# Performance work log

Measured on AMD Instinct MI355X. Metric: run time of the kernel, lower is better.

## Reference

```python
import jax, jax.numpy as jnp
import numpy as np

HEAD_DIM = 64
SCALE = HEAD_DIM ** -0.5
NEG_INF = jnp.finfo(jnp.float32).min


def setup_inputs() -> dict:
    key = jax.random.key(0)
    kq, kk, kv = jax.random.split(key, 3)
    shape = (4, 16, 2048, HEAD_DIM)  # [batch, heads, seq, head_dim]
    return {
        "q": jax.random.normal(kq, shape, dtype=jnp.float32),
        "k": jax.random.normal(kk, shape, dtype=jnp.float32),
        "v": jax.random.normal(kv, shape, dtype=jnp.float32),
    }


def reference(q, k, v):
    # similarity = QK^T * scale, shape [b, h, i, j]
    sim = jnp.einsum("bhid,bhjd->bhij", q, k) * SCALE
    seq_len = sim.shape[-1]
    # causal mask: disallow j > i
    causal = jnp.triu(jnp.ones((seq_len, seq_len), dtype=bool), k=1)
    sim = jnp.where(causal, NEG_INF, sim)
    attn = jax.nn.softmax(sim, axis=-1)
    out = jnp.einsum("bhij,bhjd->bhid", attn, v)
    return out
```

## Files before the change

### kernel.cpp

```cpp
#include <hip/hip_runtime.h>
#include <hip/hip_bf16.h>

#define SEQ 2048
#define HD 64
#define NQB (SEQ / 128)

typedef __bf16 bf16x8 __attribute__((ext_vector_type(8)));
typedef float f32x4 __attribute__((ext_vector_type(4)));
typedef float f32x16 __attribute__((ext_vector_type(16)));
typedef unsigned int u32x4 __attribute__((ext_vector_type(4)));

typedef const __attribute__((address_space(1))) void gvoid_t;
typedef __attribute__((address_space(3))) void svoid_t;

__device__ __forceinline__ void gload_lds16(const void* g, void* l) {
  __builtin_amdgcn_global_load_lds((gvoid_t*)g, (svoid_t*)l, 16, 0, 0);
}

__device__ __forceinline__ bf16x8 cvt8(const float* p) {
  float4 a = *(const float4*)p;
  float4 b = *(const float4*)(p + 4);
  bf16x8 w;
  w[0] = (__bf16)a.x; w[1] = (__bf16)a.y; w[2] = (__bf16)a.z; w[3] = (__bf16)a.w;
  w[4] = (__bf16)b.x; w[5] = (__bf16)b.y; w[6] = (__bf16)b.z; w[7] = (__bf16)b.w;
  return w;
}

__device__ __forceinline__ unsigned cvtpk_bf16(float lo, float hi) {
  unsigned r;
  asm("v_cvt_pk_bf16_f32 %0, %1, %2" : "=v"(r) : "v"(lo), "v"(hi));
  return r;
}

__device__ __forceinline__ float tmax16(const f32x16& v) {
  float a0 = fmaxf(v[0], v[1]), a1 = fmaxf(v[2], v[3]);
  float a2 = fmaxf(v[4], v[5]), a3 = fmaxf(v[6], v[7]);
  float a4 = fmaxf(v[8], v[9]), a5 = fmaxf(v[10], v[11]);
  float a6 = fmaxf(v[12], v[13]), a7 = fmaxf(v[14], v[15]);
  float b0 = fmaxf(a0, a1), b1 = fmaxf(a2, a3), b2 = fmaxf(a4, a5), b3 = fmaxf(a6, a7);
  return fmaxf(fmaxf(b0, b1), fmaxf(b2, b3));
}

__global__ void prep_kernel(const float* __restrict__ K,
                            const float* __restrict__ V,
                            unsigned short* __restrict__ Kswz,
                            unsigned short* __restrict__ Vt) {
  __shared__ __align__(16) unsigned short sT[64 * 72];
  const int t = threadIdx.x;
  const int kb = blockIdx.x;
  const int bh = blockIdx.y;
  const int j0 = kb * 64;
  const size_t ibase = (size_t)bh * SEQ * HD;

  {
    const int j = t >> 2;
    const int m = (t & 3) * 2;
    const float* src = K + ibase + (size_t)(j0 + j) * HD + m * 8;
    unsigned short* dst = Kswz + ibase + (size_t)(j0 + j) * HD;
#pragma unroll
    for (int h = 0; h < 2; ++h) {
      bf16x8 w = cvt8(src + 8 * h);
      const int c = (m + h) ^ (j & 7);
      *(bf16x8*)(dst + c * 8) = w;
    }
  }
  {
    const int jr = t >> 2;
    const int d0 = (t & 3) * 16;
    const float* vsrc = V + ibase + (size_t)(j0 + jr) * HD + d0;
#pragma unroll
    for (int h = 0; h < 4; ++h) {
      float4 a = *(const float4*)(vsrc + 4 * h);
      sT[(d0 + 4 * h + 0) * 72 + jr] = __builtin_bit_cast(unsigned short, (__bf16)a.x);
      sT[(d0 + 4 * h + 1) * 72 + jr] = __builtin_bit_cast(unsigned short, (__bf16)a.y);
      sT[(d0 + 4 * h + 2) * 72 + jr] = __builtin_bit_cast(unsigned short, (__bf16)a.z);
      sT[(d0 + 4 * h + 3) * 72 + jr] = __builtin_bit_cast(unsigned short, (__bf16)a.w);
    }
  }
  __syncthreads();
  {
#pragma unroll
    for (int p = 0; p < 2; ++p) {
      const int cid = t + 256 * p;
      const int d = cid >> 3;
      const int jj = cid & 7;
      bf16x8 w = *(const bf16x8*)(&sT[d * 72 + 8 * jj]);
      const int c = jj ^ (d & 7);
      *(bf16x8*)(Vt + (size_t)bh * HD * SEQ + (size_t)d * SEQ + j0 + c * 8) = w;
    }
  }
}

__global__ __launch_bounds__(256, 2) void fattn_kernel(
    const float* __restrict__ Q, const unsigned short* __restrict__ Kswz,
    const unsigned short* __restrict__ Vt, float* __restrict__ O) {
  __shared__ __align__(16) unsigned short sbuf[3][2 * 64 * 64];

  const int tid = threadIdx.x;
  const int wid = tid >> 6;
  const int lane = tid & 63;
  const int l31 = lane & 31;
  const int hi = lane >> 5;

  const int p = blockIdx.x;
  const int qbA = p;
  const int qbB = NQB - 1 - p;
  const int bh = blockIdx.y;

  const int i0A = qbA * 128 + wid * 32;
  const int i0B = qbB * 128 + wid * 32;
  const int igA = i0A + l31;
  const int igB = i0B + l31;

  const float* Qp = Q + (size_t)bh * SEQ * HD;
  const unsigned short* Kg = Kswz + (size_t)bh * SEQ * HD;
  const unsigned short* Vg = Vt + (size_t)bh * HD * SEQ;
  float* Op = O + (size_t)bh * SEQ * HD;

  const float qscale = 0.125f * 1.44269504088896340736f;
  bf16x8 qfA[4], qfB[4];
#pragma unroll
  for (int grp = 0; grp < 2; ++grp) {
    const float* qr = Qp + (size_t)(grp ? igB : igA) * HD + 8 * hi;
#pragma unroll
    for (int c = 0; c < 4; ++c) {
      float4 a = *(const float4*)(qr + 16 * c);
      float4 b = *(const float4*)(qr + 16 * c + 4);
      bf16x8 w;
      w[0] = (__bf16)(a.x * qscale); w[1] = (__bf16)(a.y * qscale);
      w[2] = (__bf16)(a.z * qscale); w[3] = (__bf16)(a.w * qscale);
      w[4] = (__bf16)(b.x * qscale); w[5] = (__bf16)(b.y * qscale);
      w[6] = (__bf16)(b.z * qscale); w[7] = (__bf16)(b.w * qscale);
      if (grp) qfB[c] = w; else qfA[c] = w;
    }
  }

  f32x16 z16;
#pragma unroll
  for (int r = 0; r < 16; ++r) z16[r] = 0.f;

  f32x16 oAl, oBl, oAh, oBh;
#pragma unroll
  for (int r = 0; r < 16; ++r) { oAl[r] = 0.f; oBl[r] = 0.f; oAh[r] = 0.f; oBh[r] = 0.f; }
  float mA = -1e30f, lA = 0.f, mB = -1e30f, lB = 0.f;

  const int nkb = 2 * qbB + 2;
  const int kbLowMax = 2 * qbA + 1;

  auto stage = [&](int buf, int j0s) {
    unsigned short* bK = &sbuf[buf][0];
    unsigned short* bV = &sbuf[buf][4096];
#pragma unroll
    for (int tt = 0; tt < 2; ++tt) {
      const int row = 16 * wid + 8 * tt;
      const unsigned short* gk =
          Kg + (size_t)(j0s + row + (lane >> 3)) * HD + (lane & 7) * 8;
      gload_lds16(gk, bK + row * HD);
      const unsigned short* gv =
          Vg + (size_t)(row + (lane >> 3)) * SEQ + j0s + (lane & 7) * 8;
      gload_lds16(gv, bV + row * HD);
    }
  };

  const int swz = (l31 & 7) << 4;

  stage(0, 0);
  stage(1, 64);

  for (int kb = 0; kb < nkb; ++kb) {
    const int j0 = kb * 64;
    if (kb + 1 < nkb) {
      asm volatile("s_waitcnt vmcnt(4)" ::: "memory");
    } else {
      asm volatile("s_waitcnt vmcnt(0)" ::: "memory");
    }
    __builtin_amdgcn_s_barrier();
    __builtin_amdgcn_sched_barrier(0);
    if (kb + 2 < nkb) stage((kb + 2) % 3, j0 + 128);

    const unsigned short* bK = &sbuf[kb % 3][0];
    const unsigned short* bV = &sbuf[kb % 3][4096];
    const bool lowAct = (kb <= kbLowMax);

    f32x16 sAl, sBl, sAh, sBh;

    __builtin_amdgcn_s_setprio(1);
    {
      const int boff = (16 * hi) ^ swz;
      bf16x8 kf0 = *(const bf16x8*)((const char*)bK + l31 * 128 + boff);
      bf16x8 kf1 = *(const bf16x8*)((const char*)bK + (32 + l31) * 128 + boff);
      sAh = __builtin_amdgcn_mfma_f32_32x32x16_bf16(kf0, qfB[0], z16, 0, 0, 0);
      sBh = __builtin_amdgcn_mfma_f32_32x32x16_bf16(kf1, qfB[0], z16, 0, 0, 0);
      if (lowAct) {
        sAl = __builtin_amdgcn_mfma_f32_32x32x16_bf16(kf0, qfA[0], z16, 0, 0, 0);
        sBl = __builtin_amdgcn_mfma_f32_32x32x16_bf16(kf1, qfA[0], z16, 0, 0, 0);
      } else {
        sAl = z16; sBl = z16;
      }
    }
#pragma unroll
    for (int c = 1; c < 4; ++c) {
      const int boff = (32 * c + 16 * hi) ^ swz;
      bf16x8 kf0 = *(const bf16x8*)((const char*)bK + l31 * 128 + boff);
      bf16x8 kf1 = *(const bf16x8*)((const char*)bK + (32 + l31) * 128 + boff);
      sAh = __builtin_amdgcn_mfma_f32_32x32x16_bf16(kf0, qfB[c], sAh, 0, 0, 0);
      sBh = __builtin_amdgcn_mfma_f32_32x32x16_bf16(kf1, qfB[c], sBh, 0, 0, 0);
      if (lowAct) {
        sAl = __builtin_amdgcn_mfma_f32_32x32x16_bf16(kf0, qfA[c], sAl, 0, 0, 0);
        sBl = __builtin_amdgcn_mfma_f32_32x32x16_bf16(kf1, qfA[c], sBl, 0, 0, 0);
      }
    }
    __builtin_amdgcn_s_setprio(0);

    if (j0 + 63 > i0B) {
#pragma unroll
      for (int r = 0; r < 16; ++r) {
        const int jl = j0 + (r & 3) + 8 * (r >> 2) + 4 * hi;
        sAh[r] = (jl <= igB) ? sAh[r] : -1e30f;
        sBh[r] = (jl + 32 <= igB) ? sBh[r] : -1e30f;
      }
    }
    if (lowAct && (j0 + 63 > i0A)) {
#pragma unroll
      for (int r = 0; r < 16; ++r) {
        const int jl = j0 + (r & 3) + 8 * (r >> 2) + 4 * hi;
        sAl[r] = (jl <= igA) ? sAl[r] : -1e30f;
        sBl[r] = (jl + 32 <= igA) ? sBl[r] : -1e30f;
      }
    }

    bf16x8 pfh[4], pfl[4];

#define MKFRAG(SV, BASE, DST)                                                \
    {                                                                        \
      unsigned a0 = cvtpk_bf16(SV[BASE + 0], SV[BASE + 1]);                  \
      unsigned b0 = cvtpk_bf16(SV[BASE + 4], SV[BASE + 5]);                  \
      asm("v_permlane32_swap_b32 %0, %1" : "+v"(a0), "+v"(b0));              \
      unsigned a1 = cvtpk_bf16(SV[BASE + 2], SV[BASE + 3]);                  \
      unsigned b1 = cvtpk_bf16(SV[BASE + 6], SV[BASE + 7]);                  \
      asm("v_permlane32_swap_b32 %0, %1" : "+v"(a1), "+v"(b1));              \
      u32x4 wv = {a0, a1, b0, b1};                                           \
      DST = __builtin_bit_cast(bf16x8, wv);                                  \
    }

#define SOFTMAX_FRAG(SA, SB, MRUN, LRUN, OA, OB, PFR)                        \
    {                                                                        \
      float pmax = fmaxf(tmax16(SA), tmax16(SB));                            \
      pmax = fmaxf(pmax, __shfl_xor(pmax, 32));                              \
      if (!__all(pmax - MRUN <= 10.0f)) {                                    \
        const float mn = fmaxf(MRUN, pmax);                                  \
        const float al = __builtin_amdgcn_exp2f(MRUN - mn);                  \
        MRUN = mn;                                                           \
        LRUN *= al;                                                          \
        _Pragma("unroll")                                                    \
        for (int r = 0; r < 16; ++r) { OA[r] *= al; OB[r] *= al; }           \
      }                                                                      \
      float rs0 = 0.f, rs1 = 0.f, rs2 = 0.f, rs3 = 0.f;                      \
      _Pragma("unroll")                                                      \
      for (int r = 0; r < 4; ++r) {                                          \
        SA[4 * r + 0] = __builtin_amdgcn_exp2f(SA[4 * r + 0] - MRUN);        \
        SA[4 * r + 1] = __builtin_amdgcn_exp2f(SA[4 * r + 1] - MRUN);        \
        SA[4 * r + 2] = __builtin_amdgcn_exp2f(SA[4 * r + 2] - MRUN);        \
        SA[4 * r + 3] = __builtin_amdgcn_exp2f(SA[4 * r + 3] - MRUN);        \
        rs0 += SA[4 * r + 0]; rs1 += SA[4 * r + 1];                          \
        rs2 += SA[4 * r + 2]; rs3 += SA[4 * r + 3];                          \
      }                                                                      \
      _Pragma("unroll")                                                      \
      for (int r = 0; r < 4; ++r) {                                          \
        SB[4 * r + 0] = __builtin_amdgcn_exp2f(SB[4 * r + 0] - MRUN);        \
        SB[4 * r + 1] = __builtin_amdgcn_exp2f(SB[4 * r + 1] - MRUN);        \
        SB[4 * r + 2] = __builtin_amdgcn_exp2f(SB[4 * r + 2] - MRUN);        \
        SB[4 * r + 3] = __builtin_amdgcn_exp2f(SB[4 * r + 3] - MRUN);        \
        rs0 += SB[4 * r + 0]; rs1 += SB[4 * r + 1];                          \
        rs2 += SB[4 * r + 2]; rs3 += SB[4 * r + 3];                          \
      }                                                                      \
      float rs = (rs0 + rs1) + (rs2 + rs3);                                  \
      rs += __shfl_xor(rs, 32);                                              \
      LRUN += rs;                                                            \
      MKFRAG(SA, 0, PFR[0]) MKFRAG(SA, 8, PFR[1])                            \
      MKFRAG(SB, 0, PFR[2]) MKFRAG(SB, 8, PFR[3])                            \
    }

    SOFTMAX_FRAG(sAh, sBh, mB, lB, oAh, oBh, pfh)
    if (lowAct) {
      SOFTMAX_FRAG(sAl, sBl, mA, lA, oAl, oBl, pfl)
    }
#undef SOFTMAX_FRAG
#undef MKFRAG

    __builtin_amdgcn_s_setprio(1);
    if (lowAct) {
#pragma unroll
      for (int ks = 0; ks < 4; ++ks) {
        const int vbo = (32 * ks + 16 * hi) ^ swz;
        bf16x8 vf0 = *(const bf16x8*)((const char*)bV + l31 * 128 + vbo);
        bf16x8 vf1 = *(const bf16x8*)((const char*)bV + (32 + l31) * 128 + vbo);
        oAh = __builtin_amdgcn_mfma_f32_32x32x16_bf16(vf0, pfh[ks], oAh, 0, 0, 0);
        oBh = __builtin_amdgcn_mfma_f32_32x32x16_bf16(vf1, pfh[ks], oBh, 0, 0, 0);
        oAl = __builtin_amdgcn_mfma_f32_32x32x16_bf16(vf0, pfl[ks], oAl, 0, 0, 0);
        oBl = __builtin_amdgcn_mfma_f32_32x32x16_bf16(vf1, pfl[ks], oBl, 0, 0, 0);
      }
    } else {
#pragma unroll
      for (int ks = 0; ks < 4; ++ks) {
        const int vbo = (32 * ks + 16 * hi) ^ swz;
        bf16x8 vf0 = *(const bf16x8*)((const char*)bV + l31 * 128 + vbo);
        bf16x8 vf1 = *(const bf16x8*)((const char*)bV + (32 + l31) * 128 + vbo);
        oAh = __builtin_amdgcn_mfma_f32_32x32x16_bf16(vf0, pfh[ks], oAh, 0, 0, 0);
        oBh = __builtin_amdgcn_mfma_f32_32x32x16_bf16(vf1, pfh[ks], oBh, 0, 0, 0);
      }
    }
    __builtin_amdgcn_s_setprio(0);
  }

#pragma unroll
  for (int grp = 0; grp < 2; ++grp) {
    const float inv = 1.f / (grp ? lB : lA);
    float* orow = Op + (size_t)(grp ? igB : igA) * HD;
    const f32x16& xA = grp ? oAh : oAl;
    const f32x16& xB = grp ? oBh : oBl;
#pragma unroll
    for (int q2 = 0; q2 < 4; ++q2) {
      float4 o;
      o.x = xA[4 * q2 + 0] * inv; o.y = xA[4 * q2 + 1] * inv;
      o.z = xA[4 * q2 + 2] * inv; o.w = xA[4 * q2 + 3] * inv;
      *(float4*)(orow + 8 * q2 + 4 * hi) = o;
      float4 pq;
      pq.x = xB[4 * q2 + 0] * inv; pq.y = xB[4 * q2 + 1] * inv;
      pq.z = xB[4 * q2 + 2] * inv; pq.w = xB[4 * q2 + 3] * inv;
      *(float4*)(orow + 32 + 8 * q2 + 4 * hi) = pq;
    }
  }
}

__global__ void fattn_fallback(const float* __restrict__ Q,
                               const float* __restrict__ K,
                               const float* __restrict__ V,
                               float* __restrict__ O) {
  __shared__ __align__(16) unsigned short sK[64 * 64];
  __shared__ __align__(16) unsigned short sVt[64 * 72];
  __shared__ __align__(16) unsigned short sP[4][16 * 72];

  const int tid = threadIdx.x;
  const int wid = tid >> 6;
  const int lane = tid & 63;
  const int g = lane >> 4;
  const int lx = lane & 15;

  const int qb = (int)gridDim.x - 1 - (int)blockIdx.x;
  const int bh = blockIdx.y;
  const int q0 = qb * 64;

  const size_t base = (size_t)bh * SEQ * HD;
  const float* Qp = Q + base;
  const float* Kp = K + base;
  const float* Vp = V + base;
  float* Op = O + base;

  bf16x8 qf[2];
  {
    const int row = q0 + wid * 16 + lx;
    const float* qr = Qp + (size_t)row * HD + 8 * g;
#pragma unroll
    for (int c = 0; c < 2; ++c) {
      float4 a = *(const float4*)(qr + 32 * c);
      float4 b = *(const float4*)(qr + 32 * c + 4);
      bf16x8 w;
      w[0] = (__bf16)(a.x * 0.125f); w[1] = (__bf16)(a.y * 0.125f);
      w[2] = (__bf16)(a.z * 0.125f); w[3] = (__bf16)(a.w * 0.125f);
      w[4] = (__bf16)(b.x * 0.125f); w[5] = (__bf16)(b.y * 0.125f);
      w[6] = (__bf16)(b.z * 0.125f); w[7] = (__bf16)(b.w * 0.125f);
      qf[c] = w;
    }
  }

  f32x4 acc[4];
#pragma unroll
  for (int dt = 0; dt < 4; ++dt) acc[dt] = (f32x4){0.f, 0.f, 0.f, 0.f};
  float m_run[4], l_run[4];
#pragma unroll
  for (int r = 0; r < 4; ++r) { m_run[r] = -1e30f; l_run[r] = 0.f; }

  const int iw0 = q0 + wid * 16;
  const int nkb = qb + 1;

  for (int kb = 0; kb < nkb; ++kb) {
    const int j0 = kb * 64;
    __syncthreads();
    {
      const int jr = tid >> 2;
      const int d0 = (tid & 3) * 16;
      const float* src = Kp + (size_t)(j0 + jr) * HD + d0;
#pragma unroll
      for (int h = 0; h < 2; ++h) {
        bf16x8 w = cvt8(src + 8 * h);
        const int byteoff = ((d0 + 8 * h) * 2) ^ ((jr & 7) << 4);
        *(bf16x8*)((char*)sK + jr * 128 + byteoff) = w;
      }
      const float* vsrc = Vp + (size_t)(j0 + jr) * HD + d0;
#pragma unroll
      for (int h = 0; h < 4; ++h) {
        float4 a = *(const float4*)(vsrc + 4 * h);
        sVt[(d0 + 4 * h + 0) * 72 + jr] = __builtin_bit_cast(unsigned short, (__bf16)a.x);
        sVt[(d0 + 4 * h + 1) * 72 + jr] = __builtin_bit_cast(unsigned short, (__bf16)a.y);
        sVt[(d0 + 4 * h + 2) * 72 + jr] = __builtin_bit_cast(unsigned short, (__bf16)a.z);
        sVt[(d0 + 4 * h + 3) * 72 + jr] = __builtin_bit_cast(unsigned short, (__bf16)a.w);
      }
    }
    __syncthreads();

    float s[4][4];
#pragma unroll
    for (int jt = 0; jt < 4; ++jt) {
      f32x4 c = (f32x4){0.f, 0.f, 0.f, 0.f};
#pragma unroll
      for (int cc = 0; cc < 2; ++cc) {
        const int row = jt * 16 + lx;
        const int byteoff = (16 * g + 64 * cc) ^ ((row & 7) << 4);
        bf16x8 kf = *(const bf16x8*)((const char*)sK + row * 128 + byteoff);
        c = __builtin_amdgcn_mfma_f32_16x16x32_bf16(qf[cc], kf, c, 0, 0, 0);
      }
      const int jg = j0 + jt * 16 + lx;
#pragma unroll
      for (int r = 0; r < 4; ++r) {
        const int igf = iw0 + 4 * g + r;
        s[jt][r] = (jg <= igf) ? c[r] : -1e30f;
      }
    }

#pragma unroll
    for (int r = 0; r < 4; ++r) {
      float mt = fmaxf(fmaxf(s[0][r], s[1][r]), fmaxf(s[2][r], s[3][r]));
#pragma unroll
      for (int msk = 1; msk <= 8; msk <<= 1) mt = fmaxf(mt, __shfl_xor(mt, msk));
      const float mn = fmaxf(m_run[r], mt);
      const float alpha = __expf(m_run[r] - mn);
      m_run[r] = mn;
      float rs = 0.f;
#pragma unroll
      for (int jt = 0; jt < 4; ++jt) {
        const float pv = __expf(s[jt][r] - mn);
        s[jt][r] = pv;
        rs += pv;
      }
#pragma unroll
      for (int msk = 1; msk <= 8; msk <<= 1) rs += __shfl_xor(rs, msk);
      l_run[r] = l_run[r] * alpha + rs;
#pragma unroll
      for (int dt = 0; dt < 4; ++dt) acc[dt][r] *= alpha;
    }

#pragma unroll
    for (int jt = 0; jt < 4; ++jt)
#pragma unroll
      for (int r = 0; r < 4; ++r)
        sP[wid][(4 * g + r) * 72 + jt * 16 + lx] =
            __builtin_bit_cast(unsigned short, (__bf16)s[jt][r]);
    asm volatile("s_waitcnt lgkmcnt(0)" ::: "memory");

#pragma unroll
    for (int cc = 0; cc < 2; ++cc) {
      bf16x8 pf = *(const bf16x8*)(&sP[wid][lx * 72 + 8 * g + 32 * cc]);
#pragma unroll
      for (int dt = 0; dt < 4; ++dt) {
        bf16x8 vf = *(const bf16x8*)(&sVt[(lx + 16 * dt) * 72 + 8 * g + 32 * cc]);
        acc[dt] = __builtin_amdgcn_mfma_f32_16x16x32_bf16(pf, vf, acc[dt], 0, 0, 0);
      }
    }
  }

#pragma unroll
  for (int r = 0; r < 4; ++r) {
    const float inv = 1.f / l_run[r];
    const int igf = q0 + wid * 16 + 4 * g + r;
    float* orow = Op + (size_t)igf * HD + lx;
#pragma unroll
    for (int dt = 0; dt < 4; ++dt) orow[16 * dt] = acc[dt][r] * inv;
  }
}

extern "C" void kernel_launch(void* const* d_in, const int* in_sizes, int n_in,
                              void* d_out, int out_size, void* d_ws, size_t ws_size,
                              hipStream_t stream) {
  const float* q = (const float*)d_in[0];
  const float* k = (const float*)d_in[1];
  const float* v = (const float*)d_in[2];
  float* o = (float*)d_out;

  const size_t kv_elems = (size_t)64 * SEQ * HD;
  const size_t need = 2 * kv_elems * sizeof(unsigned short);

  if (ws_size >= need) {
    unsigned short* kswz = (unsigned short*)d_ws;
    unsigned short* vt = kswz + kv_elems;
    dim3 pgrid(SEQ / 64, 64);
    prep_kernel<<<pgrid, 256, 0, stream>>>(k, v, kswz, vt);
    dim3 grid(NQB / 2, 64);
    fattn_kernel<<<grid, 256, 0, stream>>>(q, kswz, vt, o);
  } else {
    dim3 grid(SEQ / 64, 64);
    fattn_fallback<<<grid, 256, 0, stream>>>(q, k, v, o);
  }
}
```

Measured before the change: 88.88 us.

## Process two KV tiles per barrier with a four-slot LDS ring

The KV loop changes from one 64-key tile per iteration with a 3-buffer ring to two tiles per iteration with a 4-buffer ring. Each iteration waits for all outstanding loads, issues loads for the next two tiles, then processes two tiles. This halves the number of barriers and waitcnt points, at the cost of more LDS (64KB per block) and a full vmcnt(0) wait each iteration, which may lower occupancy and reduce how well loads overlap with compute.

```diff
diff --git a/kernel.cpp b/kernel.cpp
--- a/kernel.cpp
+++ b/kernel.cpp
@@ -94,7 +94,7 @@
 __global__ __launch_bounds__(256, 2) void fattn_kernel(
     const float* __restrict__ Q, const unsigned short* __restrict__ Kswz,
     const unsigned short* __restrict__ Vt, float* __restrict__ O) {
-  __shared__ __align__(16) unsigned short sbuf[3][2 * 64 * 64];
+  __shared__ __align__(16) unsigned short sbuf[4][2 * 64 * 64];
 
   const int tid = threadIdx.x;
   const int wid = tid >> 6;
@@ -144,43 +144,31 @@
   for (int r = 0; r < 16; ++r) { oAl[r] = 0.f; oBl[r] = 0.f; oAh[r] = 0.f; oBh[r] = 0.f; }
   float mA = -1e30f, lA = 0.f, mB = -1e30f, lB = 0.f;
 
-  const int nkb = 2 * qbB + 2;
-  const int kbLowMax = 2 * qbA + 1;
-
-  auto stage = [&](int buf, int j0s) {
-    unsigned short* bK = &sbuf[buf][0];
-    unsigned short* bV = &sbuf[buf][4096];
+  const int totTiles = 2 * qbB + 2;
+  const int nIter = qbB + 1;
+
+  auto stage = [&](int tile) {
+    unsigned short* base = &sbuf[0][0] + (size_t)(tile & 3) * 8192;
+    const int j0s = tile * 64;
 #pragma unroll
     for (int tt = 0; tt < 2; ++tt) {
       const int row = 16 * wid + 8 * tt;
       const unsigned short* gk =
           Kg + (size_t)(j0s + row + (lane >> 3)) * HD + (lane & 7) * 8;
-      gload_lds16(gk, bK + row * HD);
+      gload_lds16(gk, base + row * HD);
       const unsigned short* gv =
           Vg + (size_t)(row + (lane >> 3)) * SEQ + j0s + (lane & 7) * 8;
-      gload_lds16(gv, bV + row * HD);
+      gload_lds16(gv, base + 4096 + row * HD);
     }
   };
 
   const int swz = (l31 & 7) << 4;
 
-  stage(0, 0);
-  stage(1, 64);
-
-  for (int kb = 0; kb < nkb; ++kb) {
-    const int j0 = kb * 64;
-    if (kb + 1 < nkb) {
-      asm volatile("s_waitcnt vmcnt(4)" ::: "memory");
-    } else {
-      asm volatile("s_waitcnt vmcnt(0)" ::: "memory");
-    }
-    __builtin_amdgcn_s_barrier();
-    __builtin_amdgcn_sched_barrier(0);
-    if (kb + 2 < nkb) stage((kb + 2) % 3, j0 + 128);
-
-    const unsigned short* bK = &sbuf[kb % 3][0];
-    const unsigned short* bV = &sbuf[kb % 3][4096];
-    const bool lowAct = (kb <= kbLowMax);
+  auto processTile = [&](int tile, bool dual) {
+    const int j0 = tile * 64;
+    const unsigned short* base = &sbuf[0][0] + (size_t)(tile & 3) * 8192;
+    const unsigned short* bK = base;
+    const unsigned short* bV = base + 4096;
 
     f32x16 sAl, sBl, sAh, sBh;
 
@@ -191,7 +179,7 @@
       bf16x8 kf1 = *(const bf16x8*)((const char*)bK + (32 + l31) * 128 + boff);
       sAh = __builtin_amdgcn_mfma_f32_32x32x16_bf16(kf0, qfB[0], z16, 0, 0, 0);
       sBh = __builtin_amdgcn_mfma_f32_32x32x16_bf16(kf1, qfB[0], z16, 0, 0, 0);
-      if (lowAct) {
+      if (dual) {
         sAl = __builtin_amdgcn_mfma_f32_32x32x16_bf16(kf0, qfA[0], z16, 0, 0, 0);
         sBl = __builtin_amdgcn_mfma_f32_32x32x16_bf16(kf1, qfA[0], z16, 0, 0, 0);
       } else {
@@ -205,7 +193,7 @@
       bf16x8 kf1 = *(const bf16x8*)((const char*)bK + (32 + l31) * 128 + boff);
       sAh = __builtin_amdgcn_mfma_f32_32x32x16_bf16(kf0, qfB[c], sAh, 0, 0, 0);
       sBh = __builtin_amdgcn_mfma_f32_32x32x16_bf16(kf1, qfB[c], sBh, 0, 0, 0);
-      if (lowAct) {
+      if (dual) {
         sAl = __builtin_amdgcn_mfma_f32_32x32x16_bf16(kf0, qfA[c], sAl, 0, 0, 0);
         sBl = __builtin_amdgcn_mfma_f32_32x32x16_bf16(kf1, qfA[c], sBl, 0, 0, 0);
       }
@@ -220,7 +208,7 @@
         sBh[r] = (jl + 32 <= igB) ? sBh[r] : -1e30f;
       }
     }
-    if (lowAct && (j0 + 63 > i0A)) {
+    if (dual && (j0 + 63 > i0A)) {
 #pragma unroll
       for (int r = 0; r < 16; ++r) {
         const int jl = j0 + (r & 3) + 8 * (r >> 2) + 4 * hi;
@@ -282,14 +270,14 @@
     }
 
     SOFTMAX_FRAG(sAh, sBh, mB, lB, oAh, oBh, pfh)
-    if (lowAct) {
+    if (dual) {
       SOFTMAX_FRAG(sAl, sBl, mA, lA, oAl, oBl, pfl)
     }
 #undef SOFTMAX_FRAG
 #undef MKFRAG
 
     __builtin_amdgcn_s_setprio(1);
-    if (lowAct) {
+    if (dual) {
 #pragma unroll
       for (int ks = 0; ks < 4; ++ks) {
         const int vbo = (32 * ks + 16 * hi) ^ swz;
@@ -311,6 +299,23 @@
       }
     }
     __builtin_amdgcn_s_setprio(0);
+  };
+
+  stage(0);
+  stage(1);
+
+  for (int t = 0; t < nIter; ++t) {
+    asm volatile("s_waitcnt vmcnt(0)" ::: "memory");
+    __builtin_amdgcn_s_barrier();
+    __builtin_amdgcn_sched_barrier(0);
+    const int s0 = 2 * t + 2;
+    if (s0 < totTiles) {
+      stage(s0);
+      stage(s0 + 1);
+    }
+    const bool dual = (t <= qbA);
+    processTile(2 * t, dual);
+    processTile(2 * t + 1, dual);
   }
 
 #pragma unroll
```

After: 85.70 us. 3.6% less time.
